# Performance work log

Hardware: AMD Instinct MI355X
Metric: run time of the kernel (lower is better)

The kernel has to match this reference:

```python
import jax, jax.numpy as jnp
import numpy as np


def masked_softmax(v, mask, axis):
    # Faithful to the torch helper (memory_efficient=False branch):
    # softmax(v * mask), re-mask, renormalize with eps.
    m = mask.astype(v.dtype)
    r = jax.nn.softmax(v * m, axis=axis)
    r = r * m
    return r / (r.sum(axis=axis, keepdims=True) + 1e-13)


def setup_inputs() -> dict:
    key = jax.random.key(0)
    ks = jax.random.split(key, 7)
    B, L1, L2, D, A = 64, 512, 512, 512, 256
    s = 0.05  # keep tanh inputs in a non-saturated range
    return {
        "seq_features1": jax.random.normal(ks[0], (B, L1, D), jnp.float32),
        "seq_features2": jax.random.normal(ks[1], (B, L2, D), jnp.float32),
        "mask1": jnp.ones((B, L1), jnp.int32),
        "mask2": jnp.ones((B, L2), jnp.int32),
        "W": jax.random.normal(ks[2], (D, D), jnp.float32) * s,
        "Wv": jax.random.normal(ks[3], (D, A), jnp.float32) * s,
        "Wq": jax.random.normal(ks[4], (D, A), jnp.float32) * s,
        "w_hv": jax.random.normal(ks[5], (A, 1), jnp.float32) * s,
        "w_hq": jax.random.normal(ks[6], (A, 1), jnp.float32) * s,
    }


def reference(seq_features1, seq_features2, mask1, mask2, W, Wv, Wq, w_hv, w_hq):
    # C: [B, L1, L2] bilinear affinity, tanh-squashed
    C = jnp.tanh(jnp.einsum('bld,de,bme->blm', seq_features1, W, seq_features2))
    s1Wv = seq_features1 @ Wv  # [B, L1, A]
    s2Wq = seq_features2 @ Wq  # [B, L2, A]
    Hv = jnp.tanh(s1Wv + C @ s2Wq)                                  # [B, L1, A]
    Hq = jnp.tanh(s2Wq + jnp.einsum('blm,bla->bma', C, s1Wv))       # [B, L2, A]
    attn_v = masked_softmax((Hv @ w_hv)[..., 0], mask1, 1)          # [B, L1]
    attn_q = masked_softmax((Hq @ w_hq)[..., 0], mask2, 1)          # [B, L2]
    v_hat = jnp.einsum('bl,bld->bd', attn_v, seq_features1)         # [B, D]
    q_hat = jnp.einsum('bm,bmd->bd', attn_q, seq_features2)         # [B, D]
    return (v_hat, q_hat)
```

## Files before the change

kernel.cpp:

```cpp
#include <hip/hip_runtime.h>

typedef _Float16 f16;
typedef _Float16 f16x8 __attribute__((ext_vector_type(8)));
typedef _Float16 f16x4 __attribute__((ext_vector_type(4)));
typedef float f32x4 __attribute__((ext_vector_type(4)));

#define BM 128
#define BN 128
#define BK 32

__device__ __forceinline__ float fast_tanh(float x) {
    return 1.0f - 2.0f / (__expf(2.0f * x) + 1.0f);
}

__device__ __forceinline__ void ld16(const void* g, void* l) {
    __builtin_amdgcn_global_load_lds(
        (const __attribute__((address_space(1))) void*)g,
        (__attribute__((address_space(3))) void*)l, 16, 0, 0);
}

__global__ __launch_bounds__(256) void f32_to_f16_k(const float* __restrict__ in,
                                                    f16* __restrict__ out, int n4) {
    int i = blockIdx.x * 256 + threadIdx.x;
    if (i >= n4) return;
    float4 v = ((const float4*)in)[i];
    f16x4 h = {(f16)v.x, (f16)v.y, (f16)v.z, (f16)v.w};
    *(f16x4*)(out + 4L * i) = h;
}

__global__ __launch_bounds__(256) void transpose_f16_k(const float* __restrict__ in,
                                                       f16* __restrict__ out, int R, int C) {
    int i = blockIdx.x * 256 + threadIdx.x;
    if (i >= R * C) return;
    int c = i / R, r = i - c * R;
    out[i] = (f16)in[r * C + c];
}

__global__ __launch_bounds__(256) void gemm_nt(
    const f16* __restrict__ A, const f16* __restrict__ B,
    int lda, int ldb, int K,
    long sA, long sB,
    int mode,
    f16* __restrict__ Cout, int ldc, long sC,
    f16* __restrict__ CTout, int ldct, long sCT,
    const f16* __restrict__ Sadd, int ldsa, long sS,
    const float* __restrict__ wvec,
    float* __restrict__ logits, long sL)
{
    int z = blockIdx.z;
    const f16* Ab = A + (long)z * sA;
    const f16* Bb = B + (long)z * sB;
    int m0 = blockIdx.y * BM;
    int n0 = blockIdx.x * BN;
    int tid = threadIdx.x;
    int wave = tid >> 6, lane = tid & 63;
    int quad = lane >> 4, l16 = lane & 15;
    int wm = (wave >> 1) * 64, wn = (wave & 1) * 64;

    __shared__ __align__(16) char smem[32768];
    f16* T = (f16*)smem;

    f32x4 zero = {0.f, 0.f, 0.f, 0.f};
    f32x4 acc[4][4];
#pragma unroll
    for (int i = 0; i < 4; i++)
#pragma unroll
        for (int j = 0; j < 4; j++) acc[i][j] = zero;

    auto stage = [&](int buf, int k0) {
        f16* As = (f16*)(smem + buf * 16384);
        f16* Bs = (f16*)(smem + buf * 16384 + 8192);
#pragma unroll
        for (int j = 0; j < 2; j++) {
            int rbase = wave * 32 + j * 16;
            int r = rbase + (lane >> 2);
            int sw = ((lane & 3) ^ ((r >> 1) & 3)) << 3;
            ld16(Ab + (long)(m0 + r) * lda + k0 + sw, As + rbase * 32);
            ld16(Bb + (long)(n0 + r) * ldb + k0 + sw, Bs + rbase * 32);
        }
    };

    const int NK = K >> 5;
    stage(0, 0);
    for (int ki = 0; ki < NK; ki++) {
        int cur = ki & 1;
        __builtin_amdgcn_s_barrier();
        asm volatile("" ::: "memory");
        if (ki + 1 < NK) {
            stage(1 - cur, (ki + 1) << 5);
            __builtin_amdgcn_s_waitcnt(0xF74);
        } else {
            __builtin_amdgcn_s_waitcnt(0xF70);
        }
        __builtin_amdgcn_s_barrier();
        asm volatile("" ::: "memory");

        const f16* As = (const f16*)(smem + cur * 16384);
        const f16* Bs = (const f16*)(smem + cur * 16384 + 8192);
        f16x8 af[4], bfr[4];
#pragma unroll
        for (int mt = 0; mt < 4; mt++) {
            int row = wm + mt * 16 + l16;
            af[mt] = *(const f16x8*)(As + row * 32 + ((quad ^ ((row >> 1) & 3)) << 3));
        }
#pragma unroll
        for (int nt = 0; nt < 4; nt++) {
            int row = wn + nt * 16 + l16;
            bfr[nt] = *(const f16x8*)(Bs + row * 32 + ((quad ^ ((row >> 1) & 3)) << 3));
        }
#pragma unroll
        for (int mt = 0; mt < 4; mt++)
#pragma unroll
            for (int nt = 0; nt < 4; nt++)
                acc[mt][nt] = __builtin_amdgcn_mfma_f32_16x16x32_f16(af[mt], bfr[nt], acc[mt][nt], 0, 0, 0);
        asm volatile("" ::: "memory");
    }

    int gmb = m0 + wm;
    int gnb = n0 + wn;

    if (mode == 3) {
        const f16* Sb = Sadd + (long)z * sS;
        float* lg = logits + (long)z * sL;
#pragma unroll
        for (int mt = 0; mt < 4; mt++) {
            int rowb = gmb + mt * 16 + quad * 4;
            float part[4] = {0.f, 0.f, 0.f, 0.f};
#pragma unroll
            for (int nt = 0; nt < 4; nt++) {
                int col = gnb + nt * 16 + l16;
                float w = wvec[col];
#pragma unroll
                for (int r = 0; r < 4; r++) {
                    float s = (float)Sb[(long)(rowb + r) * ldsa + col];
                    part[r] += fast_tanh(s + acc[mt][nt][r]) * w;
                }
            }
#pragma unroll
            for (int off = 1; off < 16; off <<= 1) {
#pragma unroll
                for (int r = 0; r < 4; r++) part[r] += __shfl_xor(part[r], off);
            }
            if (l16 == 0) {
#pragma unroll
                for (int r = 0; r < 4; r++) atomicAdd(&lg[rowb + r], part[r]);
            }
        }
        return;
    }

    f16x4 hreg[4][4];
#pragma unroll
    for (int mt = 0; mt < 4; mt++)
#pragma unroll
        for (int nt = 0; nt < 4; nt++) {
            float v0 = acc[mt][nt][0], v1 = acc[mt][nt][1];
            float v2 = acc[mt][nt][2], v3 = acc[mt][nt][3];
            if (mode == 1) {
                v0 = fast_tanh(v0); v1 = fast_tanh(v1);
                v2 = fast_tanh(v2); v3 = fast_tanh(v3);
            }
            f16x4 hv = {(f16)v0, (f16)v1, (f16)v2, (f16)v3};
            hreg[mt][nt] = hv;
        }

    f16* Cb = Cout + (long)z * sC;
#pragma unroll
    for (int mt = 0; mt < 4; mt++) {
        int rowb = gmb + mt * 16 + quad * 4;
#pragma unroll
        for (int nt = 0; nt < 4; nt++) {
            int col = gnb + nt * 16 + l16;
#pragma unroll
            for (int r = 0; r < 4; r++)
                Cb[(long)(rowb + r) * ldc + col] = hreg[mt][nt][r];
        }
    }

    if (mode == 1 || mode == 2) {
        long bb = (mode == 2) ? (m0 >> 9) : z;
        int lr0  = (mode == 2) ? (m0 & 511) : m0;
        f16* CTb = CTout + bb * sCT;
#pragma unroll
        for (int h = 0; h < 2; h++) {
            __syncthreads();
            if ((wave & 1) == h) {
#pragma unroll
                for (int mt = 0; mt < 4; mt++) {
                    int rloc = wm + mt * 16 + quad * 4;
#pragma unroll
                    for (int nt = 0; nt < 4; nt++) {
                        int cloc = nt * 16 + l16;
                        *(f16x4*)(T + cloc * 136 + rloc) = hreg[mt][nt];
                    }
                }
            }
            __syncthreads();
#pragma unroll
            for (int i = 0; i < 4; i++) {
                int id = tid + i * 256;
                int c = id >> 4, r8 = (id & 15) * 8;
                f16x8 v = *(const f16x8*)(T + c * 136 + r8);
                *(f16x8*)(CTb + (long)(n0 + h * 64 + c) * ldct + lr0 + r8) = v;
            }
        }
    }
}

__device__ __forceinline__ float block_reduce(float v, float* red, int tid, bool is_max) {
#pragma unroll
    for (int off = 32; off >= 1; off >>= 1) {
        float o = __shfl_xor(v, off);
        v = is_max ? fmaxf(v, o) : (v + o);
    }
    if ((tid & 63) == 0) red[tid >> 6] = v;
    __syncthreads();
    float t = red[0];
#pragma unroll
    for (int i = 1; i < 8; i++) t = is_max ? fmaxf(t, red[i]) : (t + red[i]);
    __syncthreads();
    return t;
}

__global__ __launch_bounds__(512) void softmax_gather(
    const float* __restrict__ logits_v, const float* __restrict__ logits_q,
    const int* __restrict__ mask1, const int* __restrict__ mask2,
    const float* __restrict__ s1f, const float* __restrict__ s2f,
    const f16* __restrict__ s1h, const f16* __restrict__ s2h, int use_h,
    float* __restrict__ out)
{
    int b = blockIdx.x;
    int which = blockIdx.y;
    int zp = blockIdx.z;
    const float* lg = (which ? logits_q : logits_v) + (long)b * 512;
    const int*   mk = (which ? mask2 : mask1) + (long)b * 512;
    float* o = out + (long)which * 64 * 512 + (long)b * 512;

    int tid = threadIdx.x;
    __shared__ float p[512];
    __shared__ float red[8];

    float m = (float)mk[tid];
    float x = lg[tid] * m;
    float mx = block_reduce(x, red, tid, true);
    float e = __expf(x - mx);
    float S1 = block_reduce(e, red, tid, false);
    float r = (e / S1) * m;
    float S2 = block_reduce(r, red, tid, false);
    p[tid] = r / (S2 + 1e-13f);
    __syncthreads();

    float acc = 0.f;
    int l0 = zp * 128;
    if (use_h) {
        const f16* S = (which ? s2h : s1h) + (long)b * 512 * 512;
#pragma unroll 8
        for (int l = l0; l < l0 + 128; l++) acc += p[l] * (float)S[(long)l * 512 + tid];
    } else {
        const float* S = (which ? s2f : s1f) + (long)b * 512 * 512;
#pragma unroll 8
        for (int l = l0; l < l0 + 128; l++) acc += p[l] * S[(long)l * 512 + tid];
    }
    atomicAdd(&o[tid], acc);
}

extern "C" void kernel_launch(void* const* d_in, const int* in_sizes, int n_in,
                              void* d_out, int out_size, void* d_ws, size_t ws_size,
                              hipStream_t stream) {
    const float* s1  = (const float*)d_in[0];
    const float* s2  = (const float*)d_in[1];
    const int* mask1 = (const int*)d_in[2];
    const int* mask2 = (const int*)d_in[3];
    const float* W   = (const float*)d_in[4];
    const float* Wv  = (const float*)d_in[5];
    const float* Wq  = (const float*)d_in[6];
    const float* whv = (const float*)d_in[7];
    const float* whq = (const float*)d_in[8];
    float* out = (float*)d_out;

    const long Bn = 64, L = 512, D = 512, Aa = 256;
    char* ws = (char*)d_ws;
    size_t off = 0;
    auto alloc = [&](size_t bytes) -> char* {
        char* p = ws + off;
        off += (bytes + 255) & ~(size_t)255;
        return p;
    };
    f16* s1b   = (f16*)alloc(Bn * L * D * 2);
    f16* s2b   = (f16*)alloc(Bn * L * D * 2);
    f16* s1W   = (f16*)alloc(Bn * L * D * 2);
    f16* Cb    = (f16*)alloc(Bn * L * L * 2);
    f16* s1Wv  = (f16*)alloc(Bn * L * Aa * 2);
    f16* s1WvT = (f16*)alloc(Bn * L * Aa * 2);
    f16* s2Wq  = (f16*)alloc(Bn * L * Aa * 2);
    f16* s2WqT = (f16*)alloc(Bn * L * Aa * 2);
    f16* WTb   = (f16*)alloc(D * D * 2);
    f16* WvTb  = (f16*)alloc(D * Aa * 2);
    f16* WqTb  = (f16*)alloc(D * Aa * 2);
    float* logv = (float*)alloc(2 * Bn * L * 4);
    float* logq = logv + Bn * L;
    size_t base_off = off;
    f16* CTded = (f16*)alloc(Bn * L * L * 2);
    if (ws_size < base_off) return;
    int use_ded = (ws_size >= off) ? 1 : 0;
    f16* CTb = use_ded ? CTded : s1b;

    int n4 = (int)(Bn * L * D / 4);
    f32_to_f16_k<<<dim3((n4 + 255) / 256), 256, 0, stream>>>(s1, s1b, n4);
    f32_to_f16_k<<<dim3((n4 + 255) / 256), 256, 0, stream>>>(s2, s2b, n4);
    transpose_f16_k<<<dim3((int)(D * D + 255) / 256), 256, 0, stream>>>(W, WTb, (int)D, (int)D);
    transpose_f16_k<<<dim3((int)(D * Aa + 255) / 256), 256, 0, stream>>>(Wv, WvTb, (int)D, (int)Aa);
    transpose_f16_k<<<dim3((int)(D * Aa + 255) / 256), 256, 0, stream>>>(Wq, WqTb, (int)D, (int)Aa);
    hipMemsetAsync(logv, 0, 2 * Bn * L * 4, stream);
    hipMemsetAsync(out, 0, (size_t)out_size * 4, stream);

    gemm_nt<<<dim3((int)(D / BN), (int)(Bn * L / BM), 1), 256, 0, stream>>>(
        s1b, WTb, (int)D, (int)D, (int)D, 0, 0,
        0, s1W, (int)D, 0,
        nullptr, 0, 0, nullptr, 0, 0, nullptr, nullptr, 0);

    gemm_nt<<<dim3((int)(Aa / BN), (int)(Bn * L / BM), 1), 256, 0, stream>>>(
        s1b, WvTb, (int)D, (int)D, (int)D, 0, 0,
        2, s1Wv, (int)Aa, 0,
        s1WvT, (int)L, L * Aa, nullptr, 0, 0, nullptr, nullptr, 0);

    gemm_nt<<<dim3((int)(Aa / BN), (int)(Bn * L / BM), 1), 256, 0, stream>>>(
        s2b, WqTb, (int)D, (int)D, (int)D, 0, 0,
        2, s2Wq, (int)Aa, 0,
        s2WqT, (int)L, L * Aa, nullptr, 0, 0, nullptr, nullptr, 0);

    gemm_nt<<<dim3((int)(L / BN), (int)(L / BM), (int)Bn), 256, 0, stream>>>(
        s1W, s2b, (int)D, (int)D, (int)D, L * D, L * D,
        1, Cb, (int)L, L * L,
        CTb, (int)L, L * L, nullptr, 0, 0, nullptr, nullptr, 0);

    gemm_nt<<<dim3((int)(Aa / BN), (int)(L / BM), (int)Bn), 256, 0, stream>>>(
        Cb, s2WqT, (int)L, (int)L, (int)L, L * L, Aa * L,
        3, nullptr, 0, 0, nullptr, 0, 0,
        s1Wv, (int)Aa, L * Aa, whv, logv, L);

    gemm_nt<<<dim3((int)(Aa / BN), (int)(L / BM), (int)Bn), 256, 0, stream>>>(
        CTb, s1WvT, (int)L, (int)L, (int)L, L * L, Aa * L,
        3, nullptr, 0, 0, nullptr, 0, 0,
        s2Wq, (int)Aa, L * Aa, whq, logq, L);

    softmax_gather<<<dim3((int)Bn, 2, 4), 512, 0, stream>>>(
        logv, logq, mask1, mask2, s1, s2, s1b, s2b, use_ded, out);
}
```

Measured before the change: 360.0 us.

## Merge prep and GEMM launches into grouped kernels with XCD-aware block swizzle

Replaces the five conversion/transpose kernels and two memsets with a single prep kernel, and groups the independent GEMMs (s1W, s1Wv, s2Wq, and the two logit GEMMs) into single multi-job launches. It also adds a block-index remapping that spreads consecutive blocks across eight groups, apparently to match the XCD layout and improve L2 reuse, and sets launch bounds of 3 blocks per CU. The softmax gather is split over 8 chunks instead of 4 for more parallelism. This cuts launch overhead and tail effects, at the cost of hardcoded sizes and job dispatch via a struct passed by value.

```diff
diff --git a/kernel.cpp b/kernel.cpp
--- a/kernel.cpp
+++ b/kernel.cpp
@@ -7,7 +7,6 @@
 
 #define BM 128
 #define BN 128
-#define BK 32
 
 __device__ __forceinline__ float fast_tanh(float x) {
     return 1.0f - 2.0f / (__expf(2.0f * x) + 1.0f);
@@ -19,39 +18,82 @@
         (__attribute__((address_space(3))) void*)l, 16, 0, 0);
 }
 
-__global__ __launch_bounds__(256) void f32_to_f16_k(const float* __restrict__ in,
-                                                    f16* __restrict__ out, int n4) {
-    int i = blockIdx.x * 256 + threadIdx.x;
-    if (i >= n4) return;
-    float4 v = ((const float4*)in)[i];
-    f16x4 h = {(f16)v.x, (f16)v.y, (f16)v.z, (f16)v.w};
-    *(f16x4*)(out + 4L * i) = h;
-}
-
-__global__ __launch_bounds__(256) void transpose_f16_k(const float* __restrict__ in,
-                                                       f16* __restrict__ out, int R, int C) {
-    int i = blockIdx.x * 256 + threadIdx.x;
-    if (i >= R * C) return;
-    int c = i / R, r = i - c * R;
-    out[i] = (f16)in[r * C + c];
-}
-
-__global__ __launch_bounds__(256) void gemm_nt(
-    const f16* __restrict__ A, const f16* __restrict__ B,
-    int lda, int ldb, int K,
-    long sA, long sB,
-    int mode,
-    f16* __restrict__ Cout, int ldc, long sC,
-    f16* __restrict__ CTout, int ldct, long sCT,
-    const f16* __restrict__ Sadd, int ldsa, long sS,
-    const float* __restrict__ wvec,
-    float* __restrict__ logits, long sL)
+__global__ __launch_bounds__(256) void prep(
+    const float* __restrict__ s1, const float* __restrict__ s2,
+    f16* __restrict__ s1b, f16* __restrict__ s2b,
+    const float* __restrict__ W, const float* __restrict__ Wv,
+    const float* __restrict__ Wq,
+    f16* __restrict__ WTb, f16* __restrict__ WvTb, f16* __restrict__ WqTb,
+    float* __restrict__ logv, float* __restrict__ out)
 {
-    int z = blockIdx.z;
-    const f16* Ab = A + (long)z * sA;
-    const f16* Bb = B + (long)z * sB;
-    int m0 = blockIdx.y * BM;
-    int n0 = blockIdx.x * BN;
+    int bid = blockIdx.x, tid = threadIdx.x;
+    if (bid < 32768) {
+        int g = bid * 256 + tid;
+        const int F = 4194304;
+        const float* src = (g < F) ? s1 : s2;
+        f16* dst = (g < F) ? s1b : s2b;
+        int i = (g < F) ? g : g - F;
+        float4 v = ((const float4*)src)[i];
+        f16x4 h = {(f16)v.x, (f16)v.y, (f16)v.z, (f16)v.w};
+        *(f16x4*)(dst + 4L * i) = h;
+    } else if (bid < 34816) {
+        int t2 = (bid - 32768) * 256 + tid;
+        if (t2 < 262144) {
+            int c = t2 >> 9, r = t2 & 511;
+            WTb[t2] = (f16)W[r * 512 + c];
+        } else if (t2 < 393216) {
+            int i = t2 - 262144;
+            int c = i >> 9, r = i & 511;
+            WvTb[i] = (f16)Wv[r * 256 + c];
+        } else {
+            int i = t2 - 393216;
+            int c = i >> 9, r = i & 511;
+            WqTb[i] = (f16)Wq[r * 256 + c];
+        }
+    } else {
+        int t3 = (bid - 34816) * 256 + tid;
+        float4 z = {0.f, 0.f, 0.f, 0.f};
+        if (t3 < 16384) ((float4*)logv)[t3] = z;
+        else ((float4*)out)[t3 - 16384] = z;
+    }
+}
+
+struct Job {
+    const f16* A; const f16* B;
+    f16* Cout; f16* CTout;
+    const f16* Sadd;
+    const float* wvec;
+    float* logits;
+    long sA, sB, sC, sCT, sS, sL;
+    int lda, ldb, ldc, ldct, ldsa;
+    int mode, swz, gxl, K;
+};
+struct JobPack { Job j[3]; int end0, end1; };
+
+__global__ __launch_bounds__(256, 3) void gemm_multi(JobPack jp) {
+    int bid = blockIdx.x;
+    int ji = (bid < jp.end0) ? 0 : ((bid < jp.end1) ? 1 : 2);
+    const Job J = jp.j[ji];
+    int local = bid - ((ji == 0) ? 0 : ((ji == 1) ? jp.end0 : jp.end1));
+
+    int bx, by, bz;
+    if (J.swz >= 0) {
+        int tg = local >> 3;
+        bz = (local & 7) + 8 * (tg >> J.swz);
+        int t = tg & ((1 << J.swz) - 1);
+        bx = t & ((1 << J.gxl) - 1);
+        by = t >> J.gxl;
+    } else {
+        bz = 0;
+        int x = local & 7, u = local >> 3;
+        bx = u >> 5;
+        by = (x << 5) | (u & 31);
+    }
+
+    const f16* Ab = J.A + (long)bz * J.sA;
+    const f16* Bb = J.B + (long)bz * J.sB;
+    int m0 = by * BM;
+    int n0 = bx * BN;
     int tid = threadIdx.x;
     int wave = tid >> 6, lane = tid & 63;
     int quad = lane >> 4, l16 = lane & 15;
@@ -67,6 +109,7 @@
 #pragma unroll
         for (int j = 0; j < 4; j++) acc[i][j] = zero;
 
+    int lda = J.lda, ldb = J.ldb;
     auto stage = [&](int buf, int k0) {
         f16* As = (f16*)(smem + buf * 16384);
         f16* Bs = (f16*)(smem + buf * 16384 + 8192);
@@ -80,7 +123,7 @@
         }
     };
 
-    const int NK = K >> 5;
+    const int NK = J.K >> 5;
     stage(0, 0);
     for (int ki = 0; ki < NK; ki++) {
         int cur = ki & 1;
@@ -119,9 +162,9 @@
     int gmb = m0 + wm;
     int gnb = n0 + wn;
 
-    if (mode == 3) {
-        const f16* Sb = Sadd + (long)z * sS;
-        float* lg = logits + (long)z * sL;
+    if (J.mode == 3) {
+        const f16* Sb = J.Sadd + (long)bz * J.sS;
+        float* lg = J.logits + (long)bz * J.sL;
 #pragma unroll
         for (int mt = 0; mt < 4; mt++) {
             int rowb = gmb + mt * 16 + quad * 4;
@@ -129,10 +172,10 @@
 #pragma unroll
             for (int nt = 0; nt < 4; nt++) {
                 int col = gnb + nt * 16 + l16;
-                float w = wvec[col];
+                float w = J.wvec[col];
 #pragma unroll
                 for (int r = 0; r < 4; r++) {
-                    float s = (float)Sb[(long)(rowb + r) * ldsa + col];
+                    float s = (float)Sb[(long)(rowb + r) * J.ldsa + col];
                     part[r] += fast_tanh(s + acc[mt][nt][r]) * w;
                 }
             }
@@ -156,7 +199,7 @@
         for (int nt = 0; nt < 4; nt++) {
             float v0 = acc[mt][nt][0], v1 = acc[mt][nt][1];
             float v2 = acc[mt][nt][2], v3 = acc[mt][nt][3];
-            if (mode == 1) {
+            if (J.mode == 1) {
                 v0 = fast_tanh(v0); v1 = fast_tanh(v1);
                 v2 = fast_tanh(v2); v3 = fast_tanh(v3);
             }
@@ -164,7 +207,7 @@
             hreg[mt][nt] = hv;
         }
 
-    f16* Cb = Cout + (long)z * sC;
+    f16* Cb = J.Cout + (long)bz * J.sC;
 #pragma unroll
     for (int mt = 0; mt < 4; mt++) {
         int rowb = gmb + mt * 16 + quad * 4;
@@ -173,14 +216,14 @@
             int col = gnb + nt * 16 + l16;
 #pragma unroll
             for (int r = 0; r < 4; r++)
-                Cb[(long)(rowb + r) * ldc + col] = hreg[mt][nt][r];
-        }
-    }
-
-    if (mode == 1 || mode == 2) {
-        long bb = (mode == 2) ? (m0 >> 9) : z;
-        int lr0  = (mode == 2) ? (m0 & 511) : m0;
-        f16* CTb = CTout + bb * sCT;
+                Cb[(long)(rowb + r) * J.ldc + col] = hreg[mt][nt][r];
+        }
+    }
+
+    if (J.mode == 1 || J.mode == 2) {
+        long bb = (J.mode == 2) ? (m0 >> 9) : bz;
+        int lr0  = (J.mode == 2) ? (m0 & 511) : m0;
+        f16* CTb = J.CTout + bb * J.sCT;
 #pragma unroll
         for (int h = 0; h < 2; h++) {
             __syncthreads();
@@ -201,7 +244,7 @@
                 int id = tid + i * 256;
                 int c = id >> 4, r8 = (id & 15) * 8;
                 f16x8 v = *(const f16x8*)(T + c * 136 + r8);
-                *(f16x8*)(CTb + (long)(n0 + h * 64 + c) * ldct + lr0 + r8) = v;
+                *(f16x8*)(CTb + (long)(n0 + h * 64 + c) * J.ldct + lr0 + r8) = v;
             }
         }
     }
@@ -251,15 +294,15 @@
     __syncthreads();
 
     float acc = 0.f;
-    int l0 = zp * 128;
+    int l0 = zp * 64;
     if (use_h) {
         const f16* S = (which ? s2h : s1h) + (long)b * 512 * 512;
 #pragma unroll 8
-        for (int l = l0; l < l0 + 128; l++) acc += p[l] * (float)S[(long)l * 512 + tid];
+        for (int l = l0; l < l0 + 64; l++) acc += p[l] * (float)S[(long)l * 512 + tid];
     } else {
         const float* S = (which ? s2f : s1f) + (long)b * 512 * 512;
 #pragma unroll 8
-        for (int l = l0; l < l0 + 128; l++) acc += p[l] * S[(long)l * 512 + tid];
+        for (int l = l0; l < l0 + 64; l++) acc += p[l] * S[(long)l * 512 + tid];
     }
     atomicAdd(&o[tid], acc);
 }
@@ -305,45 +348,58 @@
     int use_ded = (ws_size >= off) ? 1 : 0;
     f16* CTb = use_ded ? CTded : s1b;
 
-    int n4 = (int)(Bn * L * D / 4);
-    f32_to_f16_k<<<dim3((n4 + 255) / 256), 256, 0, stream>>>(s1, s1b, n4);
-    f32_to_f16_k<<<dim3((n4 + 255) / 256), 256, 0, stream>>>(s2, s2b, n4);
-    transpose_f16_k<<<dim3((int)(D * D + 255) / 256), 256, 0, stream>>>(W, WTb, (int)D, (int)D);
-    transpose_f16_k<<<dim3((int)(D * Aa + 255) / 256), 256, 0, stream>>>(Wv, WvTb, (int)D, (int)Aa);
-    transpose_f16_k<<<dim3((int)(D * Aa + 255) / 256), 256, 0, stream>>>(Wq, WqTb, (int)D, (int)Aa);
-    hipMemsetAsync(logv, 0, 2 * Bn * L * 4, stream);
-    hipMemsetAsync(out, 0, (size_t)out_size * 4, stream);
-
-    gemm_nt<<<dim3((int)(D / BN), (int)(Bn * L / BM), 1), 256, 0, stream>>>(
-        s1b, WTb, (int)D, (int)D, (int)D, 0, 0,
-        0, s1W, (int)D, 0,
-        nullptr, 0, 0, nullptr, 0, 0, nullptr, nullptr, 0);
-
-    gemm_nt<<<dim3((int)(Aa / BN), (int)(Bn * L / BM), 1), 256, 0, stream>>>(
-        s1b, WvTb, (int)D, (int)D, (int)D, 0, 0,
-        2, s1Wv, (int)Aa, 0,
-        s1WvT, (int)L, L * Aa, nullptr, 0, 0, nullptr, nullptr, 0);
-
-    gemm_nt<<<dim3((int)(Aa / BN), (int)(Bn * L / BM), 1), 256, 0, stream>>>(
-        s2b, WqTb, (int)D, (int)D, (int)D, 0, 0,
-        2, s2Wq, (int)Aa, 0,
-        s2WqT, (int)L, L * Aa, nullptr, 0, 0, nullptr, nullptr, 0);
-
-    gemm_nt<<<dim3((int)(L / BN), (int)(L / BM), (int)Bn), 256, 0, stream>>>(
-        s1W, s2b, (int)D, (int)D, (int)D, L * D, L * D,
-        1, Cb, (int)L, L * L,
-        CTb, (int)L, L * L, nullptr, 0, 0, nullptr, nullptr, 0);
-
-    gemm_nt<<<dim3((int)(Aa / BN), (int)(L / BM), (int)Bn), 256, 0, stream>>>(
-        Cb, s2WqT, (int)L, (int)L, (int)L, L * L, Aa * L,
-        3, nullptr, 0, 0, nullptr, 0, 0,
-        s1Wv, (int)Aa, L * Aa, whv, logv, L);
-
-    gemm_nt<<<dim3((int)(Aa / BN), (int)(L / BM), (int)Bn), 256, 0, stream>>>(
-        CTb, s1WvT, (int)L, (int)L, (int)L, L * L, Aa * L,
-        3, nullptr, 0, 0, nullptr, 0, 0,
-        s2Wq, (int)Aa, L * Aa, whq, logq, L);
-
-    softmax_gather<<<dim3((int)Bn, 2, 4), 512, 0, stream>>>(
+    prep<<<dim3(34944), 256, 0, stream>>>(s1, s2, s1b, s2b, W, Wv, Wq,
+                                          WTb, WvTb, WqTb, logv, out);
+
+    Job z0{};
+
+    {
+        JobPack p{};
+        Job& a = p.j[0];
+        a.A = s1b; a.B = WTb; a.Cout = s1W;
+        a.lda = 512; a.ldb = 512; a.ldc = 512; a.K = 512;
+        a.mode = 0; a.swz = -2; a.gxl = 2;
+        Job& b = p.j[1];
+        b.A = s1b; b.B = WvTb; b.Cout = s1Wv; b.CTout = s1WvT;
+        b.lda = 512; b.ldb = 512; b.ldc = 256; b.ldct = 512; b.sCT = L * Aa;
+        b.K = 512; b.mode = 2; b.swz = -2; b.gxl = 1;
+        Job& c = p.j[2];
+        c.A = s2b; c.B = WqTb; c.Cout = s2Wq; c.CTout = s2WqT;
+        c.lda = 512; c.ldb = 512; c.ldc = 256; c.ldct = 512; c.sCT = L * Aa;
+        c.K = 512; c.mode = 2; c.swz = -2; c.gxl = 1;
+        p.end0 = 1024; p.end1 = 1536;
+        gemm_multi<<<dim3(2048), 256, 0, stream>>>(p);
+    }
+
+    {
+        JobPack p{};
+        Job& a = p.j[0];
+        a.A = s1W; a.B = s2b; a.Cout = Cb; a.CTout = CTb;
+        a.lda = 512; a.ldb = 512; a.ldc = 512; a.ldct = 512;
+        a.sA = L * D; a.sB = L * D; a.sC = L * L; a.sCT = L * L;
+        a.K = 512; a.mode = 1; a.swz = 4; a.gxl = 2;
+        p.j[1] = z0; p.j[2] = z0;
+        p.end0 = 1024; p.end1 = 1024;
+        gemm_multi<<<dim3(1024), 256, 0, stream>>>(p);
+    }
+
+    {
+        JobPack p{};
+        Job& a = p.j[0];
+        a.A = Cb; a.B = s2WqT; a.Sadd = s1Wv; a.wvec = whv; a.logits = logv;
+        a.lda = 512; a.ldb = 512; a.ldsa = 256;
+        a.sA = L * L; a.sB = Aa * L; a.sS = L * Aa; a.sL = 512;
+        a.K = 512; a.mode = 3; a.swz = 3; a.gxl = 1;
+        Job& b = p.j[1];
+        b.A = CTb; b.B = s1WvT; b.Sadd = s2Wq; b.wvec = whq; b.logits = logq;
+        b.lda = 512; b.ldb = 512; b.ldsa = 256;
+        b.sA = L * L; b.sB = Aa * L; b.sS = L * Aa; b.sL = 512;
+        b.K = 512; b.mode = 3; b.swz = 3; b.gxl = 1;
+        p.j[2] = z0;
+        p.end0 = 512; p.end1 = 1024;
+        gemm_multi<<<dim3(1024), 256, 0, stream>>>(p);
+    }
+
+    softmax_gather<<<dim3((int)Bn, 2, 8), 512, 0, stream>>>(
         logv, logq, mask1, mask2, s1, s2, s1b, s2b, use_ded, out);
 }
```

Measured after the change: 300.6 us, median of 2. -16.5%, faster.
